# Performance work log

Hardware: AMD Instinct MI355X
Metric: run time of the kernel (lower is better)

The kernel has to match this reference:

```python
import jax, jax.numpy as jnp
from jax import lax
import numpy as np

# GConv2d config (matches init_kwargs)
OUT_TRANSFORMS = 4  # rotations: 0, 90, 180, 270 degrees
STRIDE = 1
PADDING = 1


def setup_inputs() -> dict:
    key = jax.random.key(0)
    k1, k2, k3, k4 = jax.random.split(key, 4)
    B, IC_EFF, H, W = 16, 256, 64, 64   # IC_EFF = in_channels * in_transformations
    OC, K, F = 64, 4, 3                 # out_channels, num_dynamic_kernels, filter_size
    x = jax.random.normal(k1, (B, IC_EFF, H, W), dtype=jnp.float32)
    W_fc = jax.random.normal(k2, (K, IC_EFF), dtype=jnp.float32) * (1.0 / np.sqrt(IC_EFF))
    b_fc = jnp.zeros((K,), dtype=jnp.float32)
    kernel_bank = jax.random.normal(k3, (K, OC, IC_EFF, F, F), dtype=jnp.float32)
    return {"x": x, "W_fc": W_fc, "b_fc": b_fc, "kernel_bank": kernel_bank}


def reference(x, W_fc, b_fc, kernel_bank):
    B, C, H, W = x.shape
    # Dynamic routing: global average pool -> linear -> softmax over kernel bank
    pooled = x.mean(axis=(2, 3))                      # [B, C]
    coeffs = jax.nn.softmax(pooled @ W_fc.T + b_fc, axis=1)  # [B, K]
    # Sample-specific base kernels: mix of kernel bank
    base = jnp.einsum('bk,kocij->bocij', coeffs, kernel_bank)  # [B, oc, C, f, f]
    # P4 orientation expansion: rotate kernel spatially, stack along out-channels
    oriented = jnp.concatenate(
        [jnp.rot90(base, k, axes=(-2, -1)) for k in range(OUT_TRANSFORMS)], axis=1
    )  # [B, 4*oc, C, f, f]
    O, f = oriented.shape[1], oriented.shape[-1]
    # Batched per-sample conv via grouped convolution (one launch instead of B)
    xg = x.reshape(1, B * C, H, W)
    kg = oriented.reshape(B * O, C, f, f)
    out = lax.conv_general_dilated(
        xg, kg,
        window_strides=(STRIDE, STRIDE),
        padding=[(PADDING, PADDING), (PADDING, PADDING)],
        dimension_numbers=('NCHW', 'OIHW', 'NCHW'),
        feature_group_count=B,
    )  # [1, B*O, H', W']
    Ho, Wo = out.shape[-2], out.shape[-1]
    return out.reshape(B, O, Ho, Wo)
```

## Files before the change

### kernel.cpp

```cpp
#include <hip/hip_runtime.h>

#define B_  16
#define C_  256
#define O_  256

typedef short    bf16x8 __attribute__((ext_vector_type(8)));
typedef float    f32x16 __attribute__((ext_vector_type(16)));
typedef unsigned u32x4  __attribute__((ext_vector_type(4)));

#define XROW_SH  1056
#define XBC_SH   (66 * XROW_SH)
#define XT_BYTES ((size_t)B_ * 16 * XBC_SH * 2)

#define WTILE_SH 9216
#define WORP_BYTES ((size_t)B_ * 16 * 4 * WTILE_SH * 2)

#define XBUF_SH  10752
#define WT2_SH   (2 * WTILE_SH)

__device__ __forceinline__ unsigned cvtpk(float lo, float hi) {
    unsigned r;
    asm("v_cvt_pk_bf16_f32 %0, %1, %2" : "=v"(r) : "v"(lo), "v"(hi));
    return r;
}

__device__ __forceinline__ void gload16(const void* g, void* l) {
    __builtin_amdgcn_global_load_lds(
        (const __attribute__((address_space(1))) unsigned int*)g,
        (__attribute__((address_space(3))) unsigned int*)l, 16, 0, 0);
}

__global__ __launch_bounds__(256) void xprep_kernel(const float* __restrict__ x,
                                                    short* __restrict__ xT,
                                                    float* __restrict__ pooled4) {
    const int cg = blockIdx.x;
    const int b  = blockIdx.y;
    const int z  = blockIdx.z;
    const int t  = threadIdx.x;
    const int lane = t & 63, wv = t >> 6;
    const int cc = cg >> 1, lh = cg & 1;

    short* xTb = xT + (size_t)(b * 16 + cc) * XBC_SH;
    const float* xb = x + ((size_t)(b * C_ + cg * 8) << 12);

    {
        u32x4 zv = {0, 0, 0, 0};
        if (t < 32) {
            int r   = z * 16 + 1 + (t >> 1);
            int col = (t & 1) ? 65 : 0;
            *(u32x4*)&xTb[r * XROW_SH + lh * 528 + col * 8] = zv;
        }
        if (z == 0 || z == 3) {
            int row = (z == 0) ? 0 : 65;
            if (t < 66) *(u32x4*)&xTb[row * XROW_SH + lh * 528 + t * 8] = zv;
        }
    }

    float s[8] = {0.f, 0.f, 0.f, 0.f, 0.f, 0.f, 0.f, 0.f};
    const int px = lane;
#pragma unroll
    for (int r = 0; r < 4; ++r) {
        const int row = z * 16 + wv * 4 + r;
        const float* src = xb + row * 64 + px;
        float v[8];
#pragma unroll
        for (int i = 0; i < 8; ++i) { v[i] = src[(size_t)i << 12]; s[i] += v[i]; }
        u32x4 d = { cvtpk(v[0], v[1]), cvtpk(v[2], v[3]),
                    cvtpk(v[4], v[5]), cvtpk(v[6], v[7]) };
        *(u32x4*)&xTb[(row + 1) * XROW_SH + lh * 528 + (px + 1) * 8] = d;
    }

#pragma unroll
    for (int i = 0; i < 8; ++i)
#pragma unroll
        for (int off = 32; off; off >>= 1) s[i] += __shfl_xor(s[i], off, 64);

    __shared__ float pr[4][8];
    if (lane == 0) {
#pragma unroll
        for (int i = 0; i < 8; ++i) pr[wv][i] = s[i];
    }
    __syncthreads();
    if (t < 8) {
        float vv = pr[0][t] + pr[1][t] + pr[2][t] + pr[3][t];
        pooled4[(z * B_ + b) * C_ + cg * 8 + t] = vv * (1.0f / 4096.0f);
    }
}

__global__ __launch_bounds__(256) void mix_kernel(const float* __restrict__ bank,
                                                  const float* __restrict__ pooled4,
                                                  const float* __restrict__ W_fc,
                                                  const float* __restrict__ b_fc,
                                                  short* __restrict__ worp) {
    const int cc = blockIdx.x;
    const int og = blockIdx.y;
    const int t  = threadIdx.x;

    __shared__ float bankL[4][4][16][10];
    __shared__ float pl[64][4];
    __shared__ float cfs[16][4];

    for (int i = t; i < 2304; i += 256) {
        int k  = i / 576, r = i % 576;
        int oc = r / 144, r2 = r % 144;
        int c  = r2 / 9,  tap = r2 % 9;
        bankL[k][oc][c][tap] =
            bank[(((size_t)k * 64 + og * 4 + oc) * C_ + cc * 16 + c) * 9 + tap];
    }
    {
        int pair = t >> 2, seg = t & 3;
        int b = pair >> 2, k = pair & 3;
        float s = 0.f;
        for (int ci = 0; ci < 64; ++ci) {
            int c = seg * 64 + ci;
            float pv = pooled4[b * C_ + c] + pooled4[(B_ + b) * C_ + c]
                     + pooled4[(2 * B_ + b) * C_ + c] + pooled4[(3 * B_ + b) * C_ + c];
            s += pv * W_fc[k * C_ + c];
        }
        pl[pair][seg] = s;
    }
    __syncthreads();
    if (t < 64) {
        int b = t >> 2, k = t & 3;
        cfs[b][k] = pl[t][0] + pl[t][1] + pl[t][2] + pl[t][3] + b_fc[k];
    }
    __syncthreads();
    if (t < 16) {
        float l0 = cfs[t][0], l1 = cfs[t][1], l2 = cfs[t][2], l3 = cfs[t][3];
        float mx = fmaxf(fmaxf(l0, l1), fmaxf(l2, l3));
        float e0 = expf(l0 - mx), e1 = expf(l1 - mx);
        float e2 = expf(l2 - mx), e3 = expf(l3 - mx);
        float inv = 1.f / (e0 + e1 + e2 + e3);
        cfs[t][0] = e0 * inv; cfs[t][1] = e1 * inv;
        cfs[t][2] = e2 * inv; cfs[t][3] = e3 * inv;
    }
    __syncthreads();

    const int oc_l = t & 3;
    const int lhs  = (t >> 2) & 1;
    const int b    = (t >> 3) & 15;
    const int rep  = t >> 7;
    const int o64  = og * 4 + oc_l;

    const float c0 = cfs[b][0], c1 = cfs[b][1], c2 = cfs[b][2], c3 = cfs[b][3];
    float mixed[8][9];
#pragma unroll
    for (int ci = 0; ci < 8; ++ci)
#pragma unroll
        for (int tp = 0; tp < 9; ++tp)
            mixed[ci][tp] = c0 * bankL[0][oc_l][lhs * 8 + ci][tp]
                          + c1 * bankL[1][oc_l][lhs * 8 + ci][tp]
                          + c2 * bankL[2][oc_l][lhs * 8 + ci][tp]
                          + c3 * bankL[3][oc_l][lhs * 8 + ci][tp];

#define STOREOQ(OQ)                                                             \
    _Pragma("unroll")                                                           \
    for (int td = 0; td < 9; ++td) {                                            \
        const int ti = td / 3, tj = td % 3;                                     \
        int si, sj;                                                             \
        if      ((OQ) == 0) { si = ti;     sj = tj;     }                       \
        else if ((OQ) == 1) { si = tj;     sj = 2 - ti; }                       \
        else if ((OQ) == 2) { si = 2 - ti; sj = 2 - tj; }                       \
        else                { si = 2 - tj; sj = ti;     }                       \
        const int ts = si * 3 + sj;                                             \
        u32x4 d = { cvtpk(mixed[0][ts], mixed[1][ts]),                          \
                    cvtpk(mixed[2][ts], mixed[3][ts]),                          \
                    cvtpk(mixed[4][ts], mixed[5][ts]),                          \
                    cvtpk(mixed[6][ts], mixed[7][ts]) };                        \
        size_t base = ((((((size_t)b * 16 + cc) * 4 + (OQ)) * 9 + td) * 2       \
                        + lhs) * 64 + o64) * 8;                                 \
        *(u32x4*)&worp[base] = d;                                               \
    }

    if (rep == 0) { STOREOQ(0) STOREOQ(1) }
    else          { STOREOQ(2) STOREOQ(3) }
#undef STOREOQ
}

__global__ __launch_bounds__(512, 2)
void conv_mfma(const short* __restrict__ xT, const short* __restrict__ worp,
               float* __restrict__ out) {
    __shared__ short lds[2 * XBUF_SH + 2 * WT2_SH];

    const int g    = blockIdx.x;
    const int b_lo = g & 7;
    const int r_   = g >> 3;
    const int oh   = r_ & 1;
    const int rowt = (r_ >> 1) & 7;
    const int b    = ((r_ >> 4) << 3) | b_lo;
    const int y0   = rowt * 8;

    const int t    = threadIdx.x;
    const int lane = t & 63;
    const int wid  = t >> 6;
    const int wm   = wid >> 2;
    const int wn   = wid & 3;
    const int l31  = lane & 31;
    const int lh   = lane >> 5;

    const char* xsrcB = (const char*)xT
        + ((size_t)(b * 16) * XBC_SH + (size_t)y0 * XROW_SH) * 2 + lane * 16;
    const char* wsrcB = (const char*)worp
        + ((size_t)(b * 16) * 4 + oh * 2) * (WTILE_SH * 2) + lane * 16;

#define STAGE(ccc, p)                                                           \
    { const char* xs = xsrcB + (size_t)(ccc) * (XBC_SH * 2);                    \
      const char* ws = wsrcB + (size_t)(ccc) * (4 * WTILE_SH * 2);              \
      char* xd = (char*)lds + (p) * (XBUF_SH * 2);                              \
      char* wd = (char*)lds + 2 * (XBUF_SH * 2) + (p) * (WT2_SH * 2);           \
      for (int u = wid; u < 21; u += 8) gload16(xs + u * 1024, xd + u * 1024);  \
      for (int u = wid; u < 36; u += 8) gload16(ws + u * 1024, wd + u * 1024); }

#define BRD(r, s) (*(const bf16x8*)&xcur[(((r) * 2 + lh) * 66 + (s) + l31) * 8])
#define LOADROW(R, r)                                                           \
    { R[0] = BRD(r, 0);  R[1] = BRD(r, 1);  R[2] = BRD(r, 2);                   \
      R[3] = BRD(r, 32); R[4] = BRD(r, 33); R[5] = BRD(r, 34); }

#define TAPROW(i, RA, RB)                                                       \
    _Pragma("unroll")                                                           \
    for (int j = 0; j < 3; ++j) {                                               \
        const int tap = (i) * 3 + j;                                            \
        const short* wp = wcur + ((tap * 2 + lh) * 64 + l31) * 8;               \
        bf16x8 A0 = *(const bf16x8*)wp;                                         \
        bf16x8 A1 = *(const bf16x8*)(wp + 256);                                 \
        acc0[0] = __builtin_amdgcn_mfma_f32_32x32x16_bf16(A0, RA[j],     acc0[0], 0, 0, 0); \
        acc1[0] = __builtin_amdgcn_mfma_f32_32x32x16_bf16(A1, RA[j],     acc1[0], 0, 0, 0); \
        acc0[1] = __builtin_amdgcn_mfma_f32_32x32x16_bf16(A0, RA[3 + j], acc0[1], 0, 0, 0); \
        acc1[1] = __builtin_amdgcn_mfma_f32_32x32x16_bf16(A1, RA[3 + j], acc1[1], 0, 0, 0); \
        acc0[2] = __builtin_amdgcn_mfma_f32_32x32x16_bf16(A0, RB[j],     acc0[2], 0, 0, 0); \
        acc1[2] = __builtin_amdgcn_mfma_f32_32x32x16_bf16(A1, RB[j],     acc1[2], 0, 0, 0); \
        acc0[3] = __builtin_amdgcn_mfma_f32_32x32x16_bf16(A0, RB[3 + j], acc0[3], 0, 0, 0); \
        acc1[3] = __builtin_amdgcn_mfma_f32_32x32x16_bf16(A1, RB[3 + j], acc1[3], 0, 0, 0); \
    }

#define PHASE_BAR()                                                             \
    __builtin_amdgcn_sched_barrier(0);                                          \
    __builtin_amdgcn_s_barrier();                                               \
    __builtin_amdgcn_sched_barrier(0);

    f32x16 acc0[4] = {}, acc1[4] = {};

    STAGE(0, 0);
    asm volatile("s_waitcnt vmcnt(0)" ::: "memory");
    PHASE_BAR();

    for (int cc = 0; cc < 16; ++cc) {
        const int p = cc & 1;
        const short* xcur = lds + p * XBUF_SH;
        const short* wcur = lds + 2 * XBUF_SH + p * WT2_SH + wm * WTILE_SH;

        bf16x8 R0[6], R1[6];
        LOADROW(R0, 2 * wn);
        LOADROW(R1, 2 * wn + 1);
        if (cc < 15) STAGE(cc + 1, p ^ 1);
        PHASE_BAR();
        __builtin_amdgcn_s_setprio(1);
        TAPROW(0, R0, R1)
        __builtin_amdgcn_s_setprio(0);
        PHASE_BAR();
        LOADROW(R0, 2 * wn + 2);
        PHASE_BAR();
        __builtin_amdgcn_s_setprio(1);
        TAPROW(1, R1, R0)
        __builtin_amdgcn_s_setprio(0);
        PHASE_BAR();
        LOADROW(R1, 2 * wn + 3);
        PHASE_BAR();
        __builtin_amdgcn_s_setprio(1);
        TAPROW(2, R0, R1)
        __builtin_amdgcn_s_setprio(0);
        __builtin_amdgcn_sched_barrier(0);
        asm volatile("s_waitcnt vmcnt(0)" ::: "memory");
        PHASE_BAR();
    }
#undef STAGE
#undef BRD
#undef LOADROW
#undef TAPROW
#undef PHASE_BAR

#pragma unroll
    for (int pf = 0; pf < 4; ++pf) {
        const int yb  = y0 + 2 * wn + (pf >> 1);
        const int xcb = 32 * (pf & 1) + l31;
#pragma unroll
        for (int r = 0; r < 16; ++r) {
            const int orow = (r & 3) + 8 * (r >> 2) + 4 * lh;
            const int o0   = oh * 128 + wm * 64 + orow;
            __builtin_nontemporal_store(acc0[pf][r],
                &out[((size_t)(b * O_ + o0)      << 12) + yb * 64 + xcb]);
            __builtin_nontemporal_store(acc1[pf][r],
                &out[((size_t)(b * O_ + o0 + 32) << 12) + yb * 64 + xcb]);
        }
    }
}

extern "C" void kernel_launch(void* const* d_in, const int* in_sizes, int n_in,
                              void* d_out, int out_size, void* d_ws, size_t ws_size,
                              hipStream_t stream) {
    const float* x    = (const float*)d_in[0];
    const float* W_fc = (const float*)d_in[1];
    const float* b_fc = (const float*)d_in[2];
    const float* bank = (const float*)d_in[3];
    float* out = (float*)d_out;

    short* xTb     = (short*)d_ws;
    short* worp    = (short*)((char*)d_ws + XT_BYTES);
    float* pooled4 = (float*)((char*)d_ws + XT_BYTES + WORP_BYTES);

    xprep_kernel<<<dim3(32, 16, 4), 256, 0, stream>>>(x, xTb, pooled4);
    mix_kernel<<<dim3(16, 16), 256, 0, stream>>>(bank, pooled4, W_fc, b_fc, worp);
    conv_mfma<<<256, 512, 0, stream>>>(xTb, worp, out);
}
```

Measured before the change: 110.8 us.

## Use 4 waves per block each computing 128 out-channels, drop phase barriers

The conv kernel moves from 8 waves (2 along out-channels x 4 along rows) to 4 waves, each covering both 64-channel halves with 16 accumulators. A-fragments are shared across more MFMAs and x-row loads are no longer duplicated across waves. The per-tap-row block barriers and explicit vmcnt waits are replaced by one __syncthreads per channel chunk, with the next-chunk prefetch issued at the top of the loop. Each wave now holds 256 accumulator registers, which lowers occupancy and leaves fewer waves to hide LDS and global latency.

```diff
diff --git a/kernel.cpp b/kernel.cpp
--- a/kernel.cpp
+++ b/kernel.cpp
@@ -16,7 +16,7 @@
 #define WORP_BYTES ((size_t)B_ * 16 * 4 * WTILE_SH * 2)
 
 #define XBUF_SH  10752
-#define WT2_SH   (2 * WTILE_SH)
+#define WT2_SH   18432
 
 __device__ __forceinline__ unsigned cvtpk(float lo, float hi) {
     unsigned r;
@@ -177,7 +177,7 @@
 #undef STOREOQ
 }
 
-__global__ __launch_bounds__(512, 2)
+__global__ __launch_bounds__(256, 1)
 void conv_mfma(const short* __restrict__ xT, const short* __restrict__ worp,
                float* __restrict__ out) {
     __shared__ short lds[2 * XBUF_SH + 2 * WT2_SH];
@@ -192,9 +192,7 @@
 
     const int t    = threadIdx.x;
     const int lane = t & 63;
-    const int wid  = t >> 6;
-    const int wm   = wid >> 2;
-    const int wn   = wid & 3;
+    const int wn   = t >> 6;
     const int l31  = lane & 31;
     const int lh   = lane >> 5;
 
@@ -208,8 +206,8 @@
       const char* ws = wsrcB + (size_t)(ccc) * (4 * WTILE_SH * 2);              \
       char* xd = (char*)lds + (p) * (XBUF_SH * 2);                              \
       char* wd = (char*)lds + 2 * (XBUF_SH * 2) + (p) * (WT2_SH * 2);           \
-      for (int u = wid; u < 21; u += 8) gload16(xs + u * 1024, xd + u * 1024);  \
-      for (int u = wid; u < 36; u += 8) gload16(ws + u * 1024, wd + u * 1024); }
+      for (int u = wn; u < 21; u += 4) gload16(xs + u * 1024, xd + u * 1024);   \
+      for (int u = wn; u < 36; u += 4) gload16(ws + u * 1024, wd + u * 1024); }
 
 #define BRD(r, s) (*(const bf16x8*)&xcur[(((r) * 2 + lh) * 66 + (s) + l31) * 8])
 #define LOADROW(R, r)                                                           \
@@ -221,78 +219,75 @@
     for (int j = 0; j < 3; ++j) {                                               \
         const int tap = (i) * 3 + j;                                            \
         const short* wp = wcur + ((tap * 2 + lh) * 64 + l31) * 8;               \
-        bf16x8 A0 = *(const bf16x8*)wp;                                         \
-        bf16x8 A1 = *(const bf16x8*)(wp + 256);                                 \
-        acc0[0] = __builtin_amdgcn_mfma_f32_32x32x16_bf16(A0, RA[j],     acc0[0], 0, 0, 0); \
-        acc1[0] = __builtin_amdgcn_mfma_f32_32x32x16_bf16(A1, RA[j],     acc1[0], 0, 0, 0); \
-        acc0[1] = __builtin_amdgcn_mfma_f32_32x32x16_bf16(A0, RA[3 + j], acc0[1], 0, 0, 0); \
-        acc1[1] = __builtin_amdgcn_mfma_f32_32x32x16_bf16(A1, RA[3 + j], acc1[1], 0, 0, 0); \
-        acc0[2] = __builtin_amdgcn_mfma_f32_32x32x16_bf16(A0, RB[j],     acc0[2], 0, 0, 0); \
-        acc1[2] = __builtin_amdgcn_mfma_f32_32x32x16_bf16(A1, RB[j],     acc1[2], 0, 0, 0); \
-        acc0[3] = __builtin_amdgcn_mfma_f32_32x32x16_bf16(A0, RB[3 + j], acc0[3], 0, 0, 0); \
-        acc1[3] = __builtin_amdgcn_mfma_f32_32x32x16_bf16(A1, RB[3 + j], acc1[3], 0, 0, 0); \
-    }
-
-#define PHASE_BAR()                                                             \
-    __builtin_amdgcn_sched_barrier(0);                                          \
-    __builtin_amdgcn_s_barrier();                                               \
-    __builtin_amdgcn_sched_barrier(0);
-
-    f32x16 acc0[4] = {}, acc1[4] = {};
+        bf16x8 A00 = *(const bf16x8*)wp;                                        \
+        bf16x8 A01 = *(const bf16x8*)(wp + 256);                                \
+        bf16x8 A10 = *(const bf16x8*)(wp + 9216);                               \
+        bf16x8 A11 = *(const bf16x8*)(wp + 9216 + 256);                         \
+        accA[0] = __builtin_amdgcn_mfma_f32_32x32x16_bf16(A00, RA[j],     accA[0], 0, 0, 0); \
+        accA[1] = __builtin_amdgcn_mfma_f32_32x32x16_bf16(A00, RA[3 + j], accA[1], 0, 0, 0); \
+        accA[2] = __builtin_amdgcn_mfma_f32_32x32x16_bf16(A00, RB[j],     accA[2], 0, 0, 0); \
+        accA[3] = __builtin_amdgcn_mfma_f32_32x32x16_bf16(A00, RB[3 + j], accA[3], 0, 0, 0); \
+        accB[0] = __builtin_amdgcn_mfma_f32_32x32x16_bf16(A01, RA[j],     accB[0], 0, 0, 0); \
+        accB[1] = __builtin_amdgcn_mfma_f32_32x32x16_bf16(A01, RA[3 + j], accB[1], 0, 0, 0); \
+        accB[2] = __builtin_amdgcn_mfma_f32_32x32x16_bf16(A01, RB[j],     accB[2], 0, 0, 0); \
+        accB[3] = __builtin_amdgcn_mfma_f32_32x32x16_bf16(A01, RB[3 + j], accB[3], 0, 0, 0); \
+        accC[0] = __builtin_amdgcn_mfma_f32_32x32x16_bf16(A10, RA[j],     accC[0], 0, 0, 0); \
+        accC[1] = __builtin_amdgcn_mfma_f32_32x32x16_bf16(A10, RA[3 + j], accC[1], 0, 0, 0); \
+        accC[2] = __builtin_amdgcn_mfma_f32_32x32x16_bf16(A10, RB[j],     accC[2], 0, 0, 0); \
+        accC[3] = __builtin_amdgcn_mfma_f32_32x32x16_bf16(A10, RB[3 + j], accC[3], 0, 0, 0); \
+        accD[0] = __builtin_amdgcn_mfma_f32_32x32x16_bf16(A11, RA[j],     accD[0], 0, 0, 0); \
+        accD[1] = __builtin_amdgcn_mfma_f32_32x32x16_bf16(A11, RA[3 + j], accD[1], 0, 0, 0); \
+        accD[2] = __builtin_amdgcn_mfma_f32_32x32x16_bf16(A11, RB[j],     accD[2], 0, 0, 0); \
+        accD[3] = __builtin_amdgcn_mfma_f32_32x32x16_bf16(A11, RB[3 + j], accD[3], 0, 0, 0); \
+    }
+
+    f32x16 accA[4] = {}, accB[4] = {}, accC[4] = {}, accD[4] = {};
 
     STAGE(0, 0);
-    asm volatile("s_waitcnt vmcnt(0)" ::: "memory");
-    PHASE_BAR();
+    __syncthreads();
 
     for (int cc = 0; cc < 16; ++cc) {
         const int p = cc & 1;
+        if (cc < 15) STAGE(cc + 1, p ^ 1);
         const short* xcur = lds + p * XBUF_SH;
-        const short* wcur = lds + 2 * XBUF_SH + p * WT2_SH + wm * WTILE_SH;
+        const short* wcur = lds + 2 * XBUF_SH + p * WT2_SH;
 
         bf16x8 R0[6], R1[6];
+        __builtin_amdgcn_s_setprio(1);
         LOADROW(R0, 2 * wn);
         LOADROW(R1, 2 * wn + 1);
-        if (cc < 15) STAGE(cc + 1, p ^ 1);
-        PHASE_BAR();
-        __builtin_amdgcn_s_setprio(1);
         TAPROW(0, R0, R1)
-        __builtin_amdgcn_s_setprio(0);
-        PHASE_BAR();
-        LOADROW(R0, 2 * wn + 2);
-        PHASE_BAR();
-        __builtin_amdgcn_s_setprio(1);
+        LOADROW(R0, 2 * wn + 2)
         TAPROW(1, R1, R0)
-        __builtin_amdgcn_s_setprio(0);
-        PHASE_BAR();
-        LOADROW(R1, 2 * wn + 3);
-        PHASE_BAR();
-        __builtin_amdgcn_s_setprio(1);
+        LOADROW(R1, 2 * wn + 3)
         TAPROW(2, R0, R1)
         __builtin_amdgcn_s_setprio(0);
-        __builtin_amdgcn_sched_barrier(0);
-        asm volatile("s_waitcnt vmcnt(0)" ::: "memory");
-        PHASE_BAR();
+        __syncthreads();
     }
 #undef STAGE
 #undef BRD
 #undef LOADROW
 #undef TAPROW
-#undef PHASE_BAR
-
-#pragma unroll
-    for (int pf = 0; pf < 4; ++pf) {
-        const int yb  = y0 + 2 * wn + (pf >> 1);
-        const int xcb = 32 * (pf & 1) + l31;
-#pragma unroll
-        for (int r = 0; r < 16; ++r) {
-            const int orow = (r & 3) + 8 * (r >> 2) + 4 * lh;
-            const int o0   = oh * 128 + wm * 64 + orow;
-            __builtin_nontemporal_store(acc0[pf][r],
-                &out[((size_t)(b * O_ + o0)      << 12) + yb * 64 + xcb]);
-            __builtin_nontemporal_store(acc1[pf][r],
-                &out[((size_t)(b * O_ + o0 + 32) << 12) + yb * 64 + xcb]);
-        }
-    }
+
+#define EPI(ACC, Q, H)                                                          \
+    _Pragma("unroll")                                                           \
+    for (int pf = 0; pf < 4; ++pf) {                                            \
+        const int yb  = y0 + 2 * wn + (pf >> 1);                                \
+        const int xcb = 32 * (pf & 1) + l31;                                    \
+        _Pragma("unroll")                                                       \
+        for (int r = 0; r < 16; ++r) {                                          \
+            const int orow = (r & 3) + 8 * (r >> 2) + 4 * lh;                   \
+            const int o0   = oh * 128 + (Q) * 64 + (H) * 32 + orow;             \
+            __builtin_nontemporal_store(ACC[pf][r],                             \
+                &out[((size_t)(b * O_ + o0) << 12) + yb * 64 + xcb]);           \
+        }                                                                       \
+    }
+
+    EPI(accA, 0, 0)
+    EPI(accB, 0, 1)
+    EPI(accC, 1, 0)
+    EPI(accD, 1, 1)
+#undef EPI
 }
 
 extern "C" void kernel_launch(void* const* d_in, const int* in_sizes, int n_in,
@@ -310,5 +305,5 @@
 
     xprep_kernel<<<dim3(32, 16, 4), 256, 0, stream>>>(x, xTb, pooled4);
     mix_kernel<<<dim3(16, 16), 256, 0, stream>>>(bank, pooled4, W_fc, b_fc, worp);
-    conv_mfma<<<256, 512, 0, stream>>>(xTb, worp, out);
-}
+    conv_mfma<<<256, 256, 0, stream>>>(xTb, worp, out);
+}
```

Result: slower. 115.4 us (+4.2%).
